# Kernel optimization log

Measured on AMD Instinct MI355X. Metric: run time of the kernel, lower is better.

The kernel has to match this reference:

```python
import jax, jax.numpy as jnp
import numpy as np

DIM = 1024
HEADS = 8
LN_EPS = 1e-5


def _next_fast_len(n):
    # smallest 5-smooth integer >= n (matches scipy.fftpack.next_fast_len)
    while True:
        m = n
        for p in (2, 3, 5):
            while m % p == 0:
                m //= p
        if m == 1:
            return n
        n += 1


def setup_inputs() -> dict:
    key = jax.random.key(0)
    k1, k2, k3 = jax.random.split(key, 3)
    x = jax.random.normal(k1, (4, 8192, DIM), dtype=jnp.float32)
    gamma = jnp.ones((DIM,), dtype=jnp.float32)
    beta = jnp.zeros((DIM,), dtype=jnp.float32)
    alphas = jax.random.normal(k2, (HEADS,), dtype=jnp.float32)
    param_D = jax.random.normal(k3, (DIM,), dtype=jnp.float32)
    return {"x": x, "gamma": gamma, "beta": beta, "alphas": alphas, "param_D": param_D}


def reference(x, gamma, beta, alphas, param_D):
    b, L, dim = x.shape
    h = HEADS
    # LayerNorm
    mean = jnp.mean(x, axis=-1, keepdims=True)
    var = jnp.mean((x - mean) ** 2, axis=-1, keepdims=True)
    u = (x - mean) * jax.lax.rsqrt(var + LN_EPS) * gamma + beta
    residual = u * param_D
    # per-head EMA kernel K[l, h] = a_h * (1 - a_h)^(L-1-l)
    a = jax.nn.sigmoid(alphas)  # [h]
    rev_pow = jnp.arange(L - 1, -1, -1, dtype=x.dtype)  # [L]
    K = a * (1.0 - a) ** rev_pow[:, None]  # [L, h]
    # FFT causal correlation along the sequence axis
    u4 = u.reshape(b, L, h, dim // h)  # [b, L, h, d]
    fast_len = _next_fast_len(2 * L - 1)
    f_x = jnp.fft.rfft(u4, n=fast_len, axis=1)          # [b, F, h, d]
    f_w = jnp.fft.rfft(K, n=fast_len, axis=0)           # [F, h]
    f_out = f_x * jnp.conj(f_w)[None, :, :, None]
    out = jnp.fft.irfft(f_out, n=fast_len, axis=1)      # [b, fast_len, h, d]
    out = jnp.roll(out, -1, axis=1)[:, fast_len - L: fast_len]  # [b, L, h, d]
    out = out.reshape(b, L, dim)
    return out + residual
```

## Files before the change

kernel.cpp:

```cpp
#include <hip/hip_runtime.h>
#include <math.h>

#define B 4
#define SEQ 8192
#define DIM 1024
#define HEADS 8
#define NCHUNK 128
#define CLEN (SEQ / NCHUNK)
#define LN_EPS 1e-5f

__global__ void __launch_bounds__(256) pass1_kernel(
        const float* __restrict__ x,
        const float* __restrict__ gamma,
        const float* __restrict__ beta,
        const float* __restrict__ alphas,
        float2* __restrict__ stats,
        float4* __restrict__ carry) {
    const int bid   = blockIdx.x;
    const int chunk = bid & (NCHUNK - 1);
    const int b     = bid >> 7;
    const int t     = threadIdx.x;
    const int c     = t * 4;
    const int h     = c >> 7;
    const int wave  = t >> 6;
    const int lane  = t & 63;

    const float a = 1.f / (1.f + expf(-alphas[h]));
    const float r = 1.f - a;
    const float4 g  = *(const float4*)(gamma + c);
    const float4 be = *(const float4*)(beta + c);

    __shared__ float red[2][8];

    const int rowbase = b * SEQ + chunk * CLEN;
    const float4* xp = (const float4*)x + (long)rowbase * (DIM / 4) + t;

    float4 y = make_float4(0.f, 0.f, 0.f, 0.f);
    float4 xv = xp[0];

    for (int i = 0; i < CLEN; ++i) {
        const int ip = (i + 1 < CLEN) ? i + 1 : CLEN - 1;
        float4 xnext = xp[ip * (DIM / 4)];

        float s  = xv.x + xv.y + xv.z + xv.w;
        float ss = xv.x * xv.x + xv.y * xv.y + xv.z * xv.z + xv.w * xv.w;
#pragma unroll
        for (int off = 32; off > 0; off >>= 1) {
            s  += __shfl_down(s, off);
            ss += __shfl_down(ss, off);
        }
        const int par = i & 1;
        if (lane == 0) {
            red[par][wave]     = s;
            red[par][4 + wave] = ss;
        }
        __syncthreads();
        const float S    = red[par][0] + red[par][1] + red[par][2] + red[par][3];
        const float SS   = red[par][4] + red[par][5] + red[par][6] + red[par][7];
        const float mean = S * (1.f / DIM);
        const float var  = SS * (1.f / DIM) - mean * mean;
        const float rstd = rsqrtf(var + LN_EPS);
        if (t == 0) stats[rowbase + i] = make_float2(mean, rstd);

        float4 u;
        u.x = (xv.x - mean) * rstd * g.x + be.x;
        u.y = (xv.y - mean) * rstd * g.y + be.y;
        u.z = (xv.z - mean) * rstd * g.z + be.z;
        u.w = (xv.w - mean) * rstd * g.w + be.w;
        y.x = r * y.x + a * u.x;
        y.y = r * y.y + a * u.y;
        y.z = r * y.z + a * u.z;
        y.w = r * y.w + a * u.w;

        xv = xnext;
    }
    carry[(long)bid * (DIM / 4) + t] = y;
}

__global__ void carry_scan_kernel(const float* __restrict__ alphas,
                                  const float* __restrict__ carry,
                                  float* __restrict__ excl) {
    const int tid = blockIdx.x * blockDim.x + threadIdx.x;
    const int c = tid & (DIM - 1);
    const int b = tid >> 10;
    const int h = c >> 7;

    const float a = 1.f / (1.f + expf(-alphas[h]));
    const float r = 1.f - a;
    float rn = r;
#pragma unroll
    for (int q = 0; q < 6; ++q) rn = rn * rn;

    const float* cp = carry + (long)b * NCHUNK * DIM + c;
    float*       ep = excl  + (long)b * NCHUNK * DIM + c;

    float Y = 0.f;
#pragma unroll 8
    for (int k = 0; k < NCHUNK; ++k) {
        float loc = cp[(long)k * DIM];
        ep[(long)k * DIM] = Y;
        Y = rn * Y + loc;
    }
}

__global__ void __launch_bounds__(256) pass2_kernel(
        const float* __restrict__ x,
        const float2* __restrict__ stats,
        const float* __restrict__ gamma,
        const float* __restrict__ beta,
        const float* __restrict__ alphas,
        const float* __restrict__ paramD,
        const float4* __restrict__ excl,
        float4* __restrict__ out) {
    const int bid   = blockIdx.x;
    const int chunk = bid & (NCHUNK - 1);
    const int b     = bid >> 7;
    const int t     = threadIdx.x;
    const int c     = t * 4;
    const int h     = c >> 7;

    const float a = 1.f / (1.f + expf(-alphas[h]));
    const float r = 1.f - a;
    const float4 g  = *(const float4*)(gamma  + c);
    const float4 be = *(const float4*)(beta   + c);
    const float4 D  = *(const float4*)(paramD + c);

    const int rowbase = b * SEQ + chunk * CLEN;
    const float4* xp = (const float4*)x + (long)rowbase * (DIM / 4) + t;
    float4*       op = (float4*)out     + (long)rowbase * (DIM / 4) + t;

    float4 y = excl[(long)bid * (DIM / 4) + t];

#pragma unroll 4
    for (int i = 0; i < CLEN; ++i) {
        const float2 st = stats[rowbase + i];
        float4 xv = xp[i * (DIM / 4)];
        float4 u, o;
        u.x = (xv.x - st.x) * st.y * g.x + be.x;
        u.y = (xv.y - st.x) * st.y * g.y + be.y;
        u.z = (xv.z - st.x) * st.y * g.z + be.z;
        u.w = (xv.w - st.x) * st.y * g.w + be.w;
        y.x = r * y.x + a * u.x;
        y.y = r * y.y + a * u.y;
        y.z = r * y.z + a * u.z;
        y.w = r * y.w + a * u.w;
        o.x = y.x + u.x * D.x;
        o.y = y.y + u.y * D.y;
        o.z = y.z + u.z * D.z;
        o.w = y.w + u.w * D.w;
        op[i * (DIM / 4)] = o;
    }
}

extern "C" void kernel_launch(void* const* d_in, const int* in_sizes, int n_in,
                              void* d_out, int out_size, void* d_ws, size_t ws_size,
                              hipStream_t stream) {
    const float* x      = (const float*)d_in[0];
    const float* gamma  = (const float*)d_in[1];
    const float* beta   = (const float*)d_in[2];
    const float* alphas = (const float*)d_in[3];
    const float* paramD = (const float*)d_in[4];
    float* out = (float*)d_out;

    char* ws = (char*)d_ws;
    float2* stats = (float2*)ws;
    float*  carry = (float*)(ws + (1 << 18));
    float*  excl  = (float*)(ws + (1 << 18) + (1 << 21));

    pass1_kernel<<<B * NCHUNK, 256, 0, stream>>>(
        x, gamma, beta, alphas, stats, (float4*)carry);
    carry_scan_kernel<<<B * DIM / 256, 256, 0, stream>>>(alphas, carry, excl);
    pass2_kernel<<<B * NCHUNK, 256, 0, stream>>>(
        x, stats, gamma, beta, alphas, paramD, (const float4*)excl, (float4*)out);
}
```

Baseline: 283.6 us.

## Assign one wavefront per chunk, double the chunk count, and scan carries in place

Each wavefront now owns a whole chunk and holds all 1024 channels, four float4 per lane. The LayerNorm row reduction therefore becomes a pure wave-level xor shuffle with no shared memory and no per-row __syncthreads. The chunk count doubles to 256 with 32 rows each, which gives more independent sequential work. The carry scan now runs in place in 64-thread blocks, dropping the separate excl buffer, at the cost of more registers per thread and a longer serial carry scan.

Result: faster. 276.0 us (-2.7%).

```diff
diff --git a/kernel.cpp b/kernel.cpp
--- a/kernel.cpp
+++ b/kernel.cpp
@@ -5,7 +5,8 @@
 #define SEQ 8192
 #define DIM 1024
 #define HEADS 8
-#define NCHUNK 128
+#define NCHUNK 256
+#define LOG_NCHUNK 8
 #define CLEN (SEQ / NCHUNK)
 #define LN_EPS 1e-5f
 
@@ -16,89 +17,98 @@
         const float* __restrict__ alphas,
         float2* __restrict__ stats,
         float4* __restrict__ carry) {
-    const int bid   = blockIdx.x;
-    const int chunk = bid & (NCHUNK - 1);
-    const int b     = bid >> 7;
     const int t     = threadIdx.x;
-    const int c     = t * 4;
-    const int h     = c >> 7;
     const int wave  = t >> 6;
     const int lane  = t & 63;
+    const int gcid  = blockIdx.x * 4 + wave;
+    const int chunk = gcid & (NCHUNK - 1);
+    const int b     = gcid >> LOG_NCHUNK;
 
-    const float a = 1.f / (1.f + expf(-alphas[h]));
-    const float r = 1.f - a;
-    const float4 g  = *(const float4*)(gamma + c);
-    const float4 be = *(const float4*)(beta + c);
-
-    __shared__ float red[2][8];
+    float a[4], dec[4];
+    float4 g[4], be[4];
+#pragma unroll
+    for (int j = 0; j < 4; ++j) {
+        const int h = (lane >> 5) + 2 * j;
+        a[j]   = 1.f / (1.f + expf(-alphas[h]));
+        dec[j] = 1.f - a[j];
+        g[j]   = *(const float4*)(gamma + lane * 4 + j * 256);
+        be[j]  = *(const float4*)(beta  + lane * 4 + j * 256);
+    }
 
     const int rowbase = b * SEQ + chunk * CLEN;
-    const float4* xp = (const float4*)x + (long)rowbase * (DIM / 4) + t;
+    const float4* xp = (const float4*)x + (long)rowbase * (DIM / 4) + lane;
 
-    float4 y = make_float4(0.f, 0.f, 0.f, 0.f);
-    float4 xv = xp[0];
+    float4 y[4];
+#pragma unroll
+    for (int j = 0; j < 4; ++j) y[j] = make_float4(0.f, 0.f, 0.f, 0.f);
+
+    float4 xv[4];
+#pragma unroll
+    for (int j = 0; j < 4; ++j) xv[j] = xp[j * 64];
 
     for (int i = 0; i < CLEN; ++i) {
-        const int ip = (i + 1 < CLEN) ? i + 1 : CLEN - 1;
-        float4 xnext = xp[ip * (DIM / 4)];
+        const int ip = (i + 1 < CLEN) ? i + 1 : i;
+        float4 xn[4];
+#pragma unroll
+        for (int j = 0; j < 4; ++j) xn[j] = xp[ip * 256 + j * 64];
 
-        float s  = xv.x + xv.y + xv.z + xv.w;
-        float ss = xv.x * xv.x + xv.y * xv.y + xv.z * xv.z + xv.w * xv.w;
+        float s = 0.f, ss = 0.f;
+#pragma unroll
+        for (int j = 0; j < 4; ++j) {
+            s  += xv[j].x + xv[j].y + xv[j].z + xv[j].w;
+            ss += xv[j].x * xv[j].x + xv[j].y * xv[j].y
+                + xv[j].z * xv[j].z + xv[j].w * xv[j].w;
+        }
 #pragma unroll
         for (int off = 32; off > 0; off >>= 1) {
-            s  += __shfl_down(s, off);
-            ss += __shfl_down(ss, off);
+            s  += __shfl_xor(s, off);
+            ss += __shfl_xor(ss, off);
         }
-        const int par = i & 1;
-        if (lane == 0) {
-            red[par][wave]     = s;
-            red[par][4 + wave] = ss;
+        const float mean = s * (1.f / DIM);
+        const float var  = ss * (1.f / DIM) - mean * mean;
+        const float rstd = rsqrtf(var + LN_EPS);
+        if (lane == 0) stats[rowbase + i] = make_float2(mean, rstd);
+
+#pragma unroll
+        for (int j = 0; j < 4; ++j) {
+            float4 u;
+            u.x = (xv[j].x - mean) * rstd * g[j].x + be[j].x;
+            u.y = (xv[j].y - mean) * rstd * g[j].y + be[j].y;
+            u.z = (xv[j].z - mean) * rstd * g[j].z + be[j].z;
+            u.w = (xv[j].w - mean) * rstd * g[j].w + be[j].w;
+            y[j].x = dec[j] * y[j].x + a[j] * u.x;
+            y[j].y = dec[j] * y[j].y + a[j] * u.y;
+            y[j].z = dec[j] * y[j].z + a[j] * u.z;
+            y[j].w = dec[j] * y[j].w + a[j] * u.w;
+            xv[j] = xn[j];
         }
-        __syncthreads();
-        const float S    = red[par][0] + red[par][1] + red[par][2] + red[par][3];
-        const float SS   = red[par][4] + red[par][5] + red[par][6] + red[par][7];
-        const float mean = S * (1.f / DIM);
-        const float var  = SS * (1.f / DIM) - mean * mean;
-        const float rstd = rsqrtf(var + LN_EPS);
-        if (t == 0) stats[rowbase + i] = make_float2(mean, rstd);
-
-        float4 u;
-        u.x = (xv.x - mean) * rstd * g.x + be.x;
-        u.y = (xv.y - mean) * rstd * g.y + be.y;
-        u.z = (xv.z - mean) * rstd * g.z + be.z;
-        u.w = (xv.w - mean) * rstd * g.w + be.w;
-        y.x = r * y.x + a * u.x;
-        y.y = r * y.y + a * u.y;
-        y.z = r * y.z + a * u.z;
-        y.w = r * y.w + a * u.w;
-
-        xv = xnext;
     }
-    carry[(long)bid * (DIM / 4) + t] = y;
+#pragma unroll
+    for (int j = 0; j < 4; ++j)
+        carry[(long)gcid * (DIM / 4) + lane + j * 64] = y[j];
 }
 
-__global__ void carry_scan_kernel(const float* __restrict__ alphas,
-                                  const float* __restrict__ carry,
-                                  float* __restrict__ excl) {
-    const int tid = blockIdx.x * blockDim.x + threadIdx.x;
-    const int c = tid & (DIM - 1);
-    const int b = tid >> 10;
-    const int h = c >> 7;
+__global__ void __launch_bounds__(64) carry_scan_kernel(
+        const float* __restrict__ alphas,
+        float* __restrict__ carry) {
+    const int tid = blockIdx.x * 64 + threadIdx.x;
+    const int c   = tid & (DIM - 1);
+    const int b   = tid >> 10;
+    const int h   = c >> 7;
 
     const float a = 1.f / (1.f + expf(-alphas[h]));
     const float r = 1.f - a;
     float rn = r;
 #pragma unroll
-    for (int q = 0; q < 6; ++q) rn = rn * rn;
+    for (int q = 0; q < 5; ++q) rn = rn * rn;
 
-    const float* cp = carry + (long)b * NCHUNK * DIM + c;
-    float*       ep = excl  + (long)b * NCHUNK * DIM + c;
+    float* cp = carry + (long)b * NCHUNK * DIM + c;
 
     float Y = 0.f;
-#pragma unroll 8
+#pragma unroll 16
     for (int k = 0; k < NCHUNK; ++k) {
-        float loc = cp[(long)k * DIM];
-        ep[(long)k * DIM] = Y;
+        const float loc = cp[(long)k * DIM];
+        cp[(long)k * DIM] = Y;
         Y = rn * Y + loc;
     }
 }
@@ -112,43 +122,55 @@
         const float* __restrict__ paramD,
         const float4* __restrict__ excl,
         float4* __restrict__ out) {
-    const int bid   = blockIdx.x;
-    const int chunk = bid & (NCHUNK - 1);
-    const int b     = bid >> 7;
     const int t     = threadIdx.x;
-    const int c     = t * 4;
-    const int h     = c >> 7;
+    const int wave  = t >> 6;
+    const int lane  = t & 63;
+    const int gcid  = blockIdx.x * 4 + wave;
+    const int chunk = gcid & (NCHUNK - 1);
+    const int b     = gcid >> LOG_NCHUNK;
 
-    const float a = 1.f / (1.f + expf(-alphas[h]));
-    const float r = 1.f - a;
-    const float4 g  = *(const float4*)(gamma  + c);
-    const float4 be = *(const float4*)(beta   + c);
-    const float4 D  = *(const float4*)(paramD + c);
+    float a[4], dec[4];
+    float4 g[4], be[4], D[4];
+#pragma unroll
+    for (int j = 0; j < 4; ++j) {
+        const int h = (lane >> 5) + 2 * j;
+        a[j]   = 1.f / (1.f + expf(-alphas[h]));
+        dec[j] = 1.f - a[j];
+        g[j]   = *(const float4*)(gamma  + lane * 4 + j * 256);
+        be[j]  = *(const float4*)(beta   + lane * 4 + j * 256);
+        D[j]   = *(const float4*)(paramD + lane * 4 + j * 256);
+    }
 
     const int rowbase = b * SEQ + chunk * CLEN;
-    const float4* xp = (const float4*)x + (long)rowbase * (DIM / 4) + t;
-    float4*       op = (float4*)out     + (long)rowbase * (DIM / 4) + t;
+    const float4* xp = (const float4*)x + (long)rowbase * (DIM / 4) + lane;
+    float4*       op = (float4*)out     + (long)rowbase * (DIM / 4) + lane;
 
-    float4 y = excl[(long)bid * (DIM / 4) + t];
+    float4 y[4];
+#pragma unroll
+    for (int j = 0; j < 4; ++j)
+        y[j] = excl[(long)gcid * (DIM / 4) + lane + j * 64];
 
 #pragma unroll 4
     for (int i = 0; i < CLEN; ++i) {
         const float2 st = stats[rowbase + i];
-        float4 xv = xp[i * (DIM / 4)];
-        float4 u, o;
-        u.x = (xv.x - st.x) * st.y * g.x + be.x;
-        u.y = (xv.y - st.x) * st.y * g.y + be.y;
-        u.z = (xv.z - st.x) * st.y * g.z + be.z;
-        u.w = (xv.w - st.x) * st.y * g.w + be.w;
-        y.x = r * y.x + a * u.x;
-        y.y = r * y.y + a * u.y;
-        y.z = r * y.z + a * u.z;
-        y.w = r * y.w + a * u.w;
-        o.x = y.x + u.x * D.x;
-        o.y = y.y + u.y * D.y;
-        o.z = y.z + u.z * D.z;
-        o.w = y.w + u.w * D.w;
-        op[i * (DIM / 4)] = o;
+#pragma unroll
+        for (int j = 0; j < 4; ++j) {
+            const float4 xv = xp[i * 256 + j * 64];
+            float4 u, o;
+            u.x = (xv.x - st.x) * st.y * g[j].x + be[j].x;
+            u.y = (xv.y - st.x) * st.y * g[j].y + be[j].y;
+            u.z = (xv.z - st.x) * st.y * g[j].z + be[j].z;
+            u.w = (xv.w - st.x) * st.y * g[j].w + be[j].w;
+            y[j].x = dec[j] * y[j].x + a[j] * u.x;
+            y[j].y = dec[j] * y[j].y + a[j] * u.y;
+            y[j].z = dec[j] * y[j].z + a[j] * u.z;
+            y[j].w = dec[j] * y[j].w + a[j] * u.w;
+            o.x = y[j].x + u.x * D[j].x;
+            o.y = y[j].y + u.y * D[j].y;
+            o.z = y[j].z + u.z * D[j].z;
+            o.w = y[j].w + u.w * D[j].w;
+            op[i * 256 + j * 64] = o;
+        }
     }
 }
 
@@ -165,11 +187,10 @@
     char* ws = (char*)d_ws;
     float2* stats = (float2*)ws;
     float*  carry = (float*)(ws + (1 << 18));
-    float*  excl  = (float*)(ws + (1 << 18) + (1 << 21));
 
-    pass1_kernel<<<B * NCHUNK, 256, 0, stream>>>(
+    pass1_kernel<<<B * NCHUNK / 4, 256, 0, stream>>>(
         x, gamma, beta, alphas, stats, (float4*)carry);
-    carry_scan_kernel<<<B * DIM / 256, 256, 0, stream>>>(alphas, carry, excl);
-    pass2_kernel<<<B * NCHUNK, 256, 0, stream>>>(
-        x, stats, gamma, beta, alphas, paramD, (const float4*)excl, (float4*)out);
+    carry_scan_kernel<<<B * DIM / 64, 64, 0, stream>>>(alphas, carry);
+    pass2_kernel<<<B * NCHUNK / 4, 256, 0, stream>>>(
+        x, stats, gamma, beta, alphas, paramD, (const float4*)carry, (float4*)out);
 }
```
